# Kernel optimization log

Hardware: AMD Instinct MI355X
Metric: run time of the kernel (lower is better)

Reference implementation:

```python
import jax, jax.numpy as jnp
import numpy as np

N_HEADS = 12
C = 3          # per-head in/hidden/out channels (12/4)
C_PRED = 1     # predictor hidden (4/4)
BN_EPS = 1e-5
COS_EPS = 1e-8
B, H, W = 8, 512, 768


def setup_inputs() -> dict:
    key = jax.random.key(0)
    ks = jax.random.split(key, 22)
    p = lambda k, s: jax.random.normal(k, s, jnp.float32) * 0.1
    return {
        "latent1": jax.random.normal(ks[0], (B, N_HEADS, H, W), jnp.float32),
        "latent2": jax.random.normal(ks[1], (B, N_HEADS, H, W), jnp.float32),
        # projector conv1 + BN
        "W1": p(ks[2], (N_HEADS, C, C)), "b1": p(ks[3], (N_HEADS, C)),
        "g1": 1.0 + p(ks[4], (N_HEADS, C)), "be1": p(ks[5], (N_HEADS, C)),
        # projector conv2 + BN
        "W2": p(ks[6], (N_HEADS, C, C)), "b2": p(ks[7], (N_HEADS, C)),
        "g2": 1.0 + p(ks[8], (N_HEADS, C)), "be2": p(ks[9], (N_HEADS, C)),
        # projector conv3 + BN (no ReLU)
        "W3": p(ks[10], (N_HEADS, C, C)), "b3": p(ks[11], (N_HEADS, C)),
        "g3": 1.0 + p(ks[12], (N_HEADS, C)), "be3": p(ks[13], (N_HEADS, C)),
        # predictor conv1 + BN
        "W4": p(ks[14], (N_HEADS, C_PRED, C)), "b4": p(ks[15], (N_HEADS, C_PRED)),
        "g4": 1.0 + p(ks[16], (N_HEADS, C_PRED)), "be4": p(ks[17], (N_HEADS, C_PRED)),
        # predictor conv2 (no BN)
        "W5": p(ks[18], (N_HEADS, C, C_PRED)), "b5": p(ks[19], (N_HEADS, C)),
    }


def _conv1x1(x, Wk, bk):
    # x: [B, Cin, H, W'], Wk: [Cout, Cin]
    return jnp.einsum('oc,bchw->bohw', Wk, x) + bk[None, :, None, None]


def _bn(x, g, be):
    # training-mode BatchNorm2d: batch statistics over (B, H, W)
    m = x.mean(axis=(0, 2, 3), keepdims=True)
    v = x.var(axis=(0, 2, 3), keepdims=True)  # biased var, as torch BN uses
    return (x - m) * jax.lax.rsqrt(v + BN_EPS) * g[None, :, None, None] + be[None, :, None, None]


def _cos_loss(p, z):
    # -mean(cosine_similarity(p, detach(z), dim=1))
    z = jax.lax.stop_gradient(z)
    dot = jnp.sum(p * z, axis=1)
    npn = jnp.maximum(jnp.sqrt(jnp.sum(p * p, axis=1)), COS_EPS)
    nzn = jnp.maximum(jnp.sqrt(jnp.sum(z * z, axis=1)), COS_EPS)
    return -jnp.mean(dot / (npn * nzn))


def _head_loss(x1, x2, W1, b1, g1, be1, W2, b2, g2, be2, W3, b3, g3, be3,
               W4, b4, g4, be4, W5, b5):
    def proj(x):
        x = jax.nn.relu(_bn(_conv1x1(x, W1, b1), g1, be1))
        x = jax.nn.relu(_bn(_conv1x1(x, W2, b2), g2, be2))
        return _bn(_conv1x1(x, W3, b3), g3, be3)

    def pred(z):
        h = jax.nn.relu(_bn(_conv1x1(z, W4, b4), g4, be4))
        return _conv1x1(h, W5, b5)

    z1, z2 = proj(x1), proj(x2)
    p1, p2 = pred(z1), pred(z2)
    return 0.5 * (_cos_loss(p1, z2) + _cos_loss(p2, z1))


def reference(latent1, latent2, W1, b1, g1, be1, W2, b2, g2, be2,
              W3, b3, g3, be3, W4, b4, g4, be4, W5, b5):
    Bd, Cd, Hd, Wd = latent1.shape
    Wp = Wd // C
    # per-channel view [B, H, W] -> [B, 3, H, W/3]; stack heads on leading axis
    x1 = latent1.reshape(Bd, N_HEADS, C, Hd, Wp).transpose(1, 0, 2, 3, 4)
    x2 = latent2.reshape(Bd, N_HEADS, C, Hd, Wp).transpose(1, 0, 2, 3, 4)
    losses = jax.vmap(_head_loss)(x1, x2, W1, b1, g1, be1, W2, b2, g2, be2,
                                  W3, b3, g3, be3, W4, b4, g4, be4, W5, b5)
    return jnp.sum(losses)
```

## Files before the change

kernel.cpp:

```cpp
#include <hip/hip_runtime.h>
#include <math.h>


constexpr int   NH      = 12;
constexpr int   POS     = 131072;
constexpr int   NB      = 8;
constexpr long long MLL = (long long)NB * POS;
constexpr int   NG      = (int)(MLL / 4);
constexpr int   GX      = 256;
constexpr float COS_EPS = 1e-8f;

template <int K>
__device__ inline void block_reduce_to0(double (&v)[K]) {
#pragma unroll
  for (int off = 32; off > 0; off >>= 1) {
#pragma unroll
    for (int k = 0; k < K; ++k) v[k] += __shfl_down(v[k], off, 64);
  }
  __shared__ double lds[4][K];
  const int lane = threadIdx.x & 63;
  const int wv   = threadIdx.x >> 6;
  if (lane == 0) {
#pragma unroll
    for (int k = 0; k < K; ++k) lds[wv][k] = v[k];
  }
  __syncthreads();
  if (threadIdx.x == 0) {
#pragma unroll
    for (int k = 0; k < K; ++k) v[k] = lds[0][k] + lds[1][k] + lds[2][k] + lds[3][k];
  }
}

__global__ __launch_bounds__(256) void pass1_kernel(
    const float* __restrict__ x1, const float* __restrict__ x2,
    const float* __restrict__ W1, const float* __restrict__ b1,
    double* __restrict__ P1) {
  const int s = blockIdx.y;
  const int n = s >> 1;
  const float* __restrict__ X = (s & 1) ? x2 : x1;

  float w[3][3], bb[3];
#pragma unroll
  for (int o = 0; o < 3; ++o) {
#pragma unroll
    for (int c = 0; c < 3; ++c) w[o][c] = W1[n * 9 + o * 3 + c];
    bb[o] = b1[n * 3 + o];
  }

  float acc[6] = {0.f, 0.f, 0.f, 0.f, 0.f, 0.f};
  for (int g = blockIdx.x * 256 + threadIdx.x; g < NG; g += GX * 256) {
    const int b   = g >> 15;
    const int pos = (g & 32767) << 2;
    const float* base = X + (size_t)((b * NH + n) * 3) * POS + pos;
    const float4 v0 = *(const float4*)(base);
    const float4 v1 = *(const float4*)(base + POS);
    const float4 v2 = *(const float4*)(base + 2 * POS);
    const float* f0 = (const float*)&v0;
    const float* f1 = (const float*)&v1;
    const float* f2 = (const float*)&v2;
#pragma unroll
    for (int j = 0; j < 4; ++j) {
      const float X0 = f0[j], X1 = f1[j], X2 = f2[j];
#pragma unroll
      for (int o = 0; o < 3; ++o) {
        const float y = fmaf(w[o][0], X0, fmaf(w[o][1], X1, fmaf(w[o][2], X2, bb[o])));
        acc[o]     += y;
        acc[3 + o] += y * y;
      }
    }
  }

  double v[6];
#pragma unroll
  for (int k = 0; k < 6; ++k) v[k] = (double)acc[k];
  block_reduce_to0<6>(v);
  if (threadIdx.x == 0) {
    double* dst = P1 + ((size_t)s * GX + blockIdx.x) * 6;
#pragma unroll
    for (int k = 0; k < 6; ++k) dst[k] = v[k];
  }
}

__global__ __launch_bounds__(256) void pass2_kernel(
    const float* __restrict__ x1, const float* __restrict__ x2,
    const float* __restrict__ W1, const float* __restrict__ b1,
    const float* __restrict__ W2, const float* __restrict__ b2,
    const float* __restrict__ derived, double* __restrict__ P2) {
  const int s = blockIdx.y;
  const int n = s >> 1;
  const float* __restrict__ X = (s & 1) ? x2 : x1;

  float w1[3][3], bb1[3], w2[3][3], bb2[3], s1[3], t1[3];
#pragma unroll
  for (int o = 0; o < 3; ++o) {
#pragma unroll
    for (int c = 0; c < 3; ++c) {
      w1[o][c] = W1[n * 9 + o * 3 + c];
      w2[o][c] = W2[n * 9 + o * 3 + c];
    }
    bb1[o] = b1[n * 3 + o];
    bb2[o] = b2[n * 3 + o];
    s1[o]  = derived[s * 20 + o];
    t1[o]  = derived[s * 20 + 3 + o];
  }

  float acc[6] = {0.f, 0.f, 0.f, 0.f, 0.f, 0.f};
  for (int g = blockIdx.x * 256 + threadIdx.x; g < NG; g += GX * 256) {
    const int b   = g >> 15;
    const int pos = (g & 32767) << 2;
    const float* base = X + (size_t)((b * NH + n) * 3) * POS + pos;
    const float4 v0 = *(const float4*)(base);
    const float4 v1 = *(const float4*)(base + POS);
    const float4 v2 = *(const float4*)(base + 2 * POS);
    const float* f0 = (const float*)&v0;
    const float* f1 = (const float*)&v1;
    const float* f2 = (const float*)&v2;
#pragma unroll
    for (int j = 0; j < 4; ++j) {
      const float X0 = f0[j], X1 = f1[j], X2 = f2[j];
      float a[3];
#pragma unroll
      for (int o = 0; o < 3; ++o) {
        const float y = fmaf(w1[o][0], X0, fmaf(w1[o][1], X1, fmaf(w1[o][2], X2, bb1[o])));
        a[o] = fmaxf(0.f, fmaf(s1[o], y, t1[o]));
      }
#pragma unroll
      for (int o = 0; o < 3; ++o) {
        const float y2v = fmaf(w2[o][0], a[0], fmaf(w2[o][1], a[1], fmaf(w2[o][2], a[2], bb2[o])));
        acc[o]     += y2v;
        acc[3 + o] += y2v * y2v;
      }
    }
  }

  double v[6];
#pragma unroll
  for (int k = 0; k < 6; ++k) v[k] = (double)acc[k];
  block_reduce_to0<6>(v);
  if (threadIdx.x == 0) {
    double* dst = P2 + ((size_t)s * GX + blockIdx.x) * 6;
#pragma unroll
    for (int k = 0; k < 6; ++k) dst[k] = v[k];
  }
}

__global__ __launch_bounds__(256) void pass3_kernel(
    const float* __restrict__ x1, const float* __restrict__ x2,
    const float* __restrict__ W1, const float* __restrict__ b1,
    const float* __restrict__ W2, const float* __restrict__ b2,
    const float* __restrict__ W3, const float* __restrict__ b3,
    const float* __restrict__ derived, double* __restrict__ P3) {
  const int s = blockIdx.y;
  const int n = s >> 1;
  const float* __restrict__ X = (s & 1) ? x2 : x1;

  float w1[3][3], bb1[3], w2[3][3], bb2[3], w3[3][3], bb3[3];
  float s1[3], t1[3], s2[3], t2[3];
#pragma unroll
  for (int o = 0; o < 3; ++o) {
#pragma unroll
    for (int c = 0; c < 3; ++c) {
      w1[o][c] = W1[n * 9 + o * 3 + c];
      w2[o][c] = W2[n * 9 + o * 3 + c];
      w3[o][c] = W3[n * 9 + o * 3 + c];
    }
    bb1[o] = b1[n * 3 + o];
    bb2[o] = b2[n * 3 + o];
    bb3[o] = b3[n * 3 + o];
    s1[o]  = derived[s * 20 + o];
    t1[o]  = derived[s * 20 + 3 + o];
    s2[o]  = derived[s * 20 + 6 + o];
    t2[o]  = derived[s * 20 + 9 + o];
  }

  float acc[9] = {0.f, 0.f, 0.f, 0.f, 0.f, 0.f, 0.f, 0.f, 0.f};
  for (int g = blockIdx.x * 256 + threadIdx.x; g < NG; g += GX * 256) {
    const int b   = g >> 15;
    const int pos = (g & 32767) << 2;
    const float* base = X + (size_t)((b * NH + n) * 3) * POS + pos;
    const float4 v0 = *(const float4*)(base);
    const float4 v1 = *(const float4*)(base + POS);
    const float4 v2 = *(const float4*)(base + 2 * POS);
    const float* f0 = (const float*)&v0;
    const float* f1 = (const float*)&v1;
    const float* f2 = (const float*)&v2;
#pragma unroll
    for (int j = 0; j < 4; ++j) {
      const float X0 = f0[j], X1 = f1[j], X2 = f2[j];
      float a[3], a2[3], y3[3];
#pragma unroll
      for (int o = 0; o < 3; ++o) {
        const float y = fmaf(w1[o][0], X0, fmaf(w1[o][1], X1, fmaf(w1[o][2], X2, bb1[o])));
        a[o] = fmaxf(0.f, fmaf(s1[o], y, t1[o]));
      }
#pragma unroll
      for (int o = 0; o < 3; ++o) {
        const float y = fmaf(w2[o][0], a[0], fmaf(w2[o][1], a[1], fmaf(w2[o][2], a[2], bb2[o])));
        a2[o] = fmaxf(0.f, fmaf(s2[o], y, t2[o]));
      }
#pragma unroll
      for (int o = 0; o < 3; ++o) {
        y3[o] = fmaf(w3[o][0], a2[0], fmaf(w3[o][1], a2[1], fmaf(w3[o][2], a2[2], bb3[o])));
        acc[o]     += y3[o];
        acc[3 + o] += y3[o] * y3[o];
      }
      acc[6] += y3[0] * y3[1];
      acc[7] += y3[0] * y3[2];
      acc[8] += y3[1] * y3[2];
    }
  }

  double v[9];
#pragma unroll
  for (int k = 0; k < 9; ++k) v[k] = (double)acc[k];
  block_reduce_to0<9>(v);
  if (threadIdx.x == 0) {
    double* dst = P3 + ((size_t)s * GX + blockIdx.x) * 9;
#pragma unroll
    for (int k = 0; k < 9; ++k) dst[k] = v[k];
  }
}

__global__ __launch_bounds__(256) void bn_stats_reduce(
    const double* __restrict__ partials,
    const float* __restrict__ gamma, const float* __restrict__ beta,
    float* __restrict__ derived, int doff) {
  const int s = blockIdx.x;
  const int t = threadIdx.x;
  double v[6];
  const double* p = partials + ((size_t)s * GX + t) * 6;
#pragma unroll
  for (int k = 0; k < 6; ++k) v[k] = p[k];
  block_reduce_to0<6>(v);
  if (t == 0) {
    const int n = s >> 1;
#pragma unroll
    for (int c = 0; c < 3; ++c) {
      const double mean = v[c] / (double)MLL;
      const double var  = v[3 + c] / (double)MLL - mean * mean;
      const double sc   = (double)gamma[n * 3 + c] / sqrt(var + 1e-5);
      derived[s * 20 + doff + c]     = (float)sc;
      derived[s * 20 + doff + 3 + c] = (float)((double)beta[n * 3 + c] - mean * sc);
    }
  }
}

__global__ __launch_bounds__(256) void bn_stats3_reduce(
    const double* __restrict__ partials,
    const float* __restrict__ g3, const float* __restrict__ be3,
    const float* __restrict__ W4, const float* __restrict__ b4,
    const float* __restrict__ g4, const float* __restrict__ be4,
    float* __restrict__ derived) {
  const int s = blockIdx.x;
  const int t = threadIdx.x;
  double v[9];
  const double* p = partials + ((size_t)s * GX + t) * 9;
#pragma unroll
  for (int k = 0; k < 9; ++k) v[k] = p[k];
  block_reduce_to0<9>(v);
  if (t == 0) {
    const int n = s >> 1;
    double mean[3] = {v[0] / (double)MLL, v[1] / (double)MLL, v[2] / (double)MLL};
    double E[3][3];
    E[0][0] = v[3] / (double)MLL;
    E[1][1] = v[4] / (double)MLL;
    E[2][2] = v[5] / (double)MLL;
    E[0][1] = E[1][0] = v[6] / (double)MLL;
    E[0][2] = E[2][0] = v[7] / (double)MLL;
    E[1][2] = E[2][1] = v[8] / (double)MLL;
    double cov[3][3];
    for (int i = 0; i < 3; ++i)
      for (int j = 0; j < 3; ++j) cov[i][j] = E[i][j] - mean[i] * mean[j];

    double s3[3], t3[3];
    for (int c = 0; c < 3; ++c) {
      s3[c] = (double)g3[n * 3 + c] / sqrt(cov[c][c] + 1e-5);
      t3[c] = (double)be3[n * 3 + c] - mean[c] * s3[c];
      derived[s * 20 + 12 + c] = (float)s3[c];
      derived[s * 20 + 15 + c] = (float)t3[c];
    }
    double u[3], dd = (double)b4[n];
    for (int c = 0; c < 3; ++c) {
      u[c] = (double)W4[n * 3 + c] * s3[c];
      dd += (double)W4[n * 3 + c] * t3[c];
    }
    double m4 = dd;
    for (int c = 0; c < 3; ++c) m4 += u[c] * mean[c];
    double v4 = 0.0;
    for (int i = 0; i < 3; ++i)
      for (int j = 0; j < 3; ++j) v4 += u[i] * u[j] * cov[i][j];
    const double s4 = (double)g4[n] / sqrt(v4 + 1e-5);
    derived[s * 20 + 18] = (float)s4;
    derived[s * 20 + 19] = (float)((double)be4[n] - m4 * s4);
  }
}

__device__ inline void fwd_chain(
    const float w1[3][3], const float bb1[3],
    const float w2[3][3], const float bb2[3],
    const float w3[3][3], const float bb3[3],
    const float w4[3], float b4s, const float w5[3], const float b5v[3],
    const float* __restrict__ S,
    float X0, float X1, float X2, float z[3], float p[3]) {
  float a[3], a2[3];
#pragma unroll
  for (int o = 0; o < 3; ++o) {
    const float y = fmaf(w1[o][0], X0, fmaf(w1[o][1], X1, fmaf(w1[o][2], X2, bb1[o])));
    a[o] = fmaxf(0.f, fmaf(S[o], y, S[3 + o]));
  }
#pragma unroll
  for (int o = 0; o < 3; ++o) {
    const float y = fmaf(w2[o][0], a[0], fmaf(w2[o][1], a[1], fmaf(w2[o][2], a[2], bb2[o])));
    a2[o] = fmaxf(0.f, fmaf(S[6 + o], y, S[9 + o]));
  }
  float y4 = b4s;
#pragma unroll
  for (int o = 0; o < 3; ++o) {
    const float y = fmaf(w3[o][0], a2[0], fmaf(w3[o][1], a2[1], fmaf(w3[o][2], a2[2], bb3[o])));
    z[o] = fmaf(S[12 + o], y, S[15 + o]);
    y4 = fmaf(w4[o], z[o], y4);
  }
  const float h = fmaxf(0.f, fmaf(S[18], y4, S[19]));
#pragma unroll
  for (int o = 0; o < 3; ++o) p[o] = fmaf(w5[o], h, b5v[o]);
}

__global__ __launch_bounds__(256) void pass_loss_kernel(
    const float* __restrict__ x1, const float* __restrict__ x2,
    const float* __restrict__ W1, const float* __restrict__ b1,
    const float* __restrict__ W2, const float* __restrict__ b2,
    const float* __restrict__ W3, const float* __restrict__ b3,
    const float* __restrict__ W4, const float* __restrict__ b4,
    const float* __restrict__ W5, const float* __restrict__ b5,
    const float* __restrict__ derived, double* __restrict__ PL) {
  const int n = blockIdx.y;

  float w1[3][3], bb1[3], w2[3][3], bb2[3], w3[3][3], bb3[3];
  float w4[3], b4s, w5[3], b5v[3];
#pragma unroll
  for (int o = 0; o < 3; ++o) {
#pragma unroll
    for (int c = 0; c < 3; ++c) {
      w1[o][c] = W1[n * 9 + o * 3 + c];
      w2[o][c] = W2[n * 9 + o * 3 + c];
      w3[o][c] = W3[n * 9 + o * 3 + c];
    }
    bb1[o] = b1[n * 3 + o];
    bb2[o] = b2[n * 3 + o];
    bb3[o] = b3[n * 3 + o];
    w4[o]  = W4[n * 3 + o];
    w5[o]  = W5[n * 3 + o];
    b5v[o] = b5[n * 3 + o];
  }
  b4s = b4[n];

  float S0[20], S1[20];
#pragma unroll
  for (int k = 0; k < 20; ++k) {
    S0[k] = derived[(n * 2 + 0) * 20 + k];
    S1[k] = derived[(n * 2 + 1) * 20 + k];
  }

  float acc = 0.f;
  for (int g = blockIdx.x * 256 + threadIdx.x; g < NG; g += GX * 256) {
    const int b   = g >> 15;
    const int pos = (g & 32767) << 2;
    const size_t off = (size_t)((b * NH + n) * 3) * POS + pos;
    const float4 u0 = *(const float4*)(x1 + off);
    const float4 u1 = *(const float4*)(x1 + off + POS);
    const float4 u2 = *(const float4*)(x1 + off + 2 * POS);
    const float4 q0 = *(const float4*)(x2 + off);
    const float4 q1 = *(const float4*)(x2 + off + POS);
    const float4 q2 = *(const float4*)(x2 + off + 2 * POS);
    const float* a0 = (const float*)&u0;
    const float* a1 = (const float*)&u1;
    const float* a2p = (const float*)&u2;
    const float* c0 = (const float*)&q0;
    const float* c1 = (const float*)&q1;
    const float* c2 = (const float*)&q2;
#pragma unroll
    for (int j = 0; j < 4; ++j) {
      float z1[3], p1[3], z2[3], p2[3];
      fwd_chain(w1, bb1, w2, bb2, w3, bb3, w4, b4s, w5, b5v, S0,
                a0[j], a1[j], a2p[j], z1, p1);
      fwd_chain(w1, bb1, w2, bb2, w3, bb3, w4, b4s, w5, b5v, S1,
                c0[j], c1[j], c2[j], z2, p2);

      const float d12 = p1[0] * z2[0] + p1[1] * z2[1] + p1[2] * z2[2];
      const float pp1 = p1[0] * p1[0] + p1[1] * p1[1] + p1[2] * p1[2];
      const float zz2 = z2[0] * z2[0] + z2[1] * z2[1] + z2[2] * z2[2];
      const float c12 = d12 / (fmaxf(sqrtf(pp1), COS_EPS) * fmaxf(sqrtf(zz2), COS_EPS));

      const float d21 = p2[0] * z1[0] + p2[1] * z1[1] + p2[2] * z1[2];
      const float pp2 = p2[0] * p2[0] + p2[1] * p2[1] + p2[2] * p2[2];
      const float zz1 = z1[0] * z1[0] + z1[1] * z1[1] + z1[2] * z1[2];
      const float c21 = d21 / (fmaxf(sqrtf(pp2), COS_EPS) * fmaxf(sqrtf(zz1), COS_EPS));

      acc += c12 + c21;
    }
  }

  double v[1] = {(double)acc};
  block_reduce_to0<1>(v);
  if (threadIdx.x == 0) PL[(size_t)n * GX + blockIdx.x] = v[0];
}

__global__ __launch_bounds__(256) void finalize_kernel(
    const double* __restrict__ PL, float* __restrict__ out) {
  double v[1] = {0.0};
#pragma unroll
  for (int h = 0; h < NH; ++h) v[0] += PL[(size_t)h * GX + threadIdx.x];
  block_reduce_to0<1>(v);
  if (threadIdx.x == 0) out[0] = (float)(-0.5 * v[0] / (double)MLL);
}

extern "C" void kernel_launch(void* const* d_in, const int* in_sizes, int n_in,
                              void* d_out, int out_size, void* d_ws, size_t ws_size,
                              hipStream_t stream) {
  const float* x1  = (const float*)d_in[0];
  const float* x2  = (const float*)d_in[1];
  const float* W1  = (const float*)d_in[2];
  const float* b1  = (const float*)d_in[3];
  const float* g1  = (const float*)d_in[4];
  const float* be1 = (const float*)d_in[5];
  const float* W2  = (const float*)d_in[6];
  const float* b2  = (const float*)d_in[7];
  const float* g2  = (const float*)d_in[8];
  const float* be2 = (const float*)d_in[9];
  const float* W3  = (const float*)d_in[10];
  const float* b3  = (const float*)d_in[11];
  const float* g3  = (const float*)d_in[12];
  const float* be3 = (const float*)d_in[13];
  const float* W4  = (const float*)d_in[14];
  const float* b4  = (const float*)d_in[15];
  const float* g4  = (const float*)d_in[16];
  const float* be4 = (const float*)d_in[17];
  const float* W5  = (const float*)d_in[18];
  const float* b5  = (const float*)d_in[19];

  double* dws = (double*)d_ws;
  double* P1 = dws;
  double* P2 = dws + 24 * GX * 6;
  double* P3 = dws + 2 * 24 * GX * 6;
  double* PL = dws + 2 * 24 * GX * 6 + 24 * GX * 9;
  float* derived = (float*)(dws + 2 * 24 * GX * 6 + 24 * GX * 9 + NH * GX);

  const dim3 blk(256);
  pass1_kernel<<<dim3(GX, 24), blk, 0, stream>>>(x1, x2, W1, b1, P1);
  bn_stats_reduce<<<24, 256, 0, stream>>>(P1, g1, be1, derived, 0);
  pass2_kernel<<<dim3(GX, 24), blk, 0, stream>>>(x1, x2, W1, b1, W2, b2, derived, P2);
  bn_stats_reduce<<<24, 256, 0, stream>>>(P2, g2, be2, derived, 6);
  pass3_kernel<<<dim3(GX, 24), blk, 0, stream>>>(x1, x2, W1, b1, W2, b2, W3, b3, derived, P3);
  bn_stats3_reduce<<<24, 256, 0, stream>>>(P3, g3, be3, W4, b4, g4, be4, derived);
  pass_loss_kernel<<<dim3(GX, NH), blk, 0, stream>>>(x1, x2, W1, b1, W2, b2, W3, b3,
                                                     W4, b4, W5, b5, derived, PL);
  finalize_kernel<<<1, 256, 0, stream>>>(PL, (float*)d_out);
}
```

Before: 536.7 us.

## Cache inputs as bf16 in workspace and derive layer-1 BN stats analytically

The first pass now accumulates the input channel means and covariances and computes the BN1 statistics analytically from W1. It also writes a bf16 copy of both inputs into the workspace when the workspace is large enough. Passes B, C and D then read the half-size bf16 copy instead of the fp32 inputs, cutting memory traffic in the three later passes. The grid is remapped to contiguous per-(batch, head) chunks. In exchange it adds a bf16 write pass and bf16 rounding error in the later BN statistics and the loss, plus a large workspace requirement.

After: 511.4 us. 1.05x faster.

```diff
diff --git a/kernel.cpp b/kernel.cpp
--- a/kernel.cpp
+++ b/kernel.cpp
@@ -1,14 +1,23 @@
 #include <hip/hip_runtime.h>
 #include <math.h>
 
+
+typedef unsigned short ushort_t;
+typedef unsigned int uint_t;
 
 constexpr int   NH      = 12;
 constexpr int   POS     = 131072;
 constexpr int   NB      = 8;
 constexpr long long MLL = (long long)NB * POS;
-constexpr int   NG      = (int)(MLL / 4);
-constexpr int   GX      = 256;
+constexpr int   CSPAN   = POS / 16;
+constexpr int   SBLK    = 128;
+constexpr int   NTOT    = NB * NH * 3 * POS;
 constexpr float COS_EPS = 1e-8f;
+
+constexpr size_t XB_BYTES   = (size_t)NTOT * 2;
+constexpr size_t DBL_COUNT  = (size_t)24 * SBLK * 9 + (size_t)24 * SBLK * 6 +
+                              (size_t)24 * SBLK * 9 + (size_t)12 * SBLK;
+constexpr size_t NEED_BYTES = 2 * XB_BYTES + DBL_COUNT * 8 + 480 * 4;
 
 template <int K>
 __device__ inline void block_reduce_to0(double (&v)[K]) {
@@ -31,64 +40,145 @@
   }
 }
 
-__global__ __launch_bounds__(256) void pass1_kernel(
+__device__ inline uint_t pack2bf(float lo, float hi) {
+  uint_t ul = __float_as_uint(lo);
+  uint_t uh = __float_as_uint(hi);
+  ul = ul + 0x7FFFu + ((ul >> 16) & 1u);
+  uh = uh + 0x7FFFu + ((uh >> 16) & 1u);
+  return (ul >> 16) | (uh & 0xFFFF0000u);
+}
+
+__device__ inline void unpack8(const uint4 v, float (&f)[8]) {
+  const uint_t w0 = v.x, w1 = v.y, w2 = v.z, w3 = v.w;
+  f[0] = __uint_as_float(w0 << 16); f[1] = __uint_as_float(w0 & 0xFFFF0000u);
+  f[2] = __uint_as_float(w1 << 16); f[3] = __uint_as_float(w1 & 0xFFFF0000u);
+  f[4] = __uint_as_float(w2 << 16); f[5] = __uint_as_float(w2 & 0xFFFF0000u);
+  f[6] = __uint_as_float(w3 << 16); f[7] = __uint_as_float(w3 & 0xFFFF0000u);
+}
+
+template <bool BF16>
+__device__ inline void load_ch3(const float* __restrict__ X,
+                                const ushort_t* __restrict__ XB,
+                                size_t eoff, float (&f)[3][8]) {
+#pragma unroll
+  for (int c = 0; c < 3; ++c) {
+    const size_t a = eoff + (size_t)c * POS;
+    if constexpr (BF16) {
+      const uint4 v = *(const uint4*)(XB + a);
+      unpack8(v, f[c]);
+    } else {
+      const float4 u0 = *(const float4*)(X + a);
+      const float4 u1 = *(const float4*)(X + a + 4);
+      f[c][0] = u0.x; f[c][1] = u0.y; f[c][2] = u0.z; f[c][3] = u0.w;
+      f[c][4] = u1.x; f[c][5] = u1.y; f[c][6] = u1.z; f[c][7] = u1.w;
+    }
+  }
+}
+
+template <bool STORE>
+__global__ __launch_bounds__(256) void passA_kernel(
     const float* __restrict__ x1, const float* __restrict__ x2,
-    const float* __restrict__ W1, const float* __restrict__ b1,
-    double* __restrict__ P1) {
-  const int s = blockIdx.y;
+    ushort_t* __restrict__ xb1, ushort_t* __restrict__ xb2,
+    double* __restrict__ P0) {
+  const int u = blockIdx.y;
+  const int s = u % 24;
+  const int b = u / 24;
   const int n = s >> 1;
   const float* __restrict__ X = (s & 1) ? x2 : x1;
-
-  float w[3][3], bb[3];
-#pragma unroll
-  for (int o = 0; o < 3; ++o) {
-#pragma unroll
-    for (int c = 0; c < 3; ++c) w[o][c] = W1[n * 9 + o * 3 + c];
-    bb[o] = b1[n * 3 + o];
-  }
-
-  float acc[6] = {0.f, 0.f, 0.f, 0.f, 0.f, 0.f};
-  for (int g = blockIdx.x * 256 + threadIdx.x; g < NG; g += GX * 256) {
-    const int b   = g >> 15;
-    const int pos = (g & 32767) << 2;
-    const float* base = X + (size_t)((b * NH + n) * 3) * POS + pos;
-    const float4 v0 = *(const float4*)(base);
-    const float4 v1 = *(const float4*)(base + POS);
-    const float4 v2 = *(const float4*)(base + 2 * POS);
-    const float* f0 = (const float*)&v0;
-    const float* f1 = (const float*)&v1;
-    const float* f2 = (const float*)&v2;
+  ushort_t* __restrict__ XB = (s & 1) ? xb2 : xb1;
+  const size_t off0 = (size_t)((b * NH + n) * 3) * POS + (size_t)blockIdx.x * CSPAN;
+
+  float acc[9] = {0.f, 0.f, 0.f, 0.f, 0.f, 0.f, 0.f, 0.f, 0.f};
+#pragma unroll
+  for (int i = 0; i < 8; ++i) {
+    const int idx = i * 1024 + threadIdx.x * 4;
+    float4 v[3];
+#pragma unroll
+    for (int c = 0; c < 3; ++c)
+      v[c] = *(const float4*)(X + off0 + (size_t)c * POS + idx);
+    if constexpr (STORE) {
+#pragma unroll
+      for (int c = 0; c < 3; ++c) {
+        uint2 h;
+        h.x = pack2bf(v[c].x, v[c].y);
+        h.y = pack2bf(v[c].z, v[c].w);
+        *(uint2*)(XB + off0 + (size_t)c * POS + idx) = h;
+      }
+    }
+    const float* f0 = (const float*)&v[0];
+    const float* f1 = (const float*)&v[1];
+    const float* f2 = (const float*)&v[2];
 #pragma unroll
     for (int j = 0; j < 4; ++j) {
       const float X0 = f0[j], X1 = f1[j], X2 = f2[j];
-#pragma unroll
-      for (int o = 0; o < 3; ++o) {
-        const float y = fmaf(w[o][0], X0, fmaf(w[o][1], X1, fmaf(w[o][2], X2, bb[o])));
-        acc[o]     += y;
-        acc[3 + o] += y * y;
-      }
-    }
-  }
-
-  double v[6];
-#pragma unroll
-  for (int k = 0; k < 6; ++k) v[k] = (double)acc[k];
-  block_reduce_to0<6>(v);
+      acc[0] += X0;      acc[1] += X1;      acc[2] += X2;
+      acc[3] += X0 * X0; acc[4] += X1 * X1; acc[5] += X2 * X2;
+      acc[6] += X0 * X1; acc[7] += X0 * X2; acc[8] += X1 * X2;
+    }
+  }
+
+  double v9[9];
+#pragma unroll
+  for (int k = 0; k < 9; ++k) v9[k] = (double)acc[k];
+  block_reduce_to0<9>(v9);
   if (threadIdx.x == 0) {
-    double* dst = P1 + ((size_t)s * GX + blockIdx.x) * 6;
-#pragma unroll
-    for (int k = 0; k < 6; ++k) dst[k] = v[k];
-  }
-}
-
-__global__ __launch_bounds__(256) void pass2_kernel(
+    double* dst = P0 + ((size_t)s * SBLK + b * 16 + blockIdx.x) * 9;
+#pragma unroll
+    for (int k = 0; k < 9; ++k) dst[k] = v9[k];
+  }
+}
+
+__global__ __launch_bounds__(256) void bn_statsA_kernel(
+    const double* __restrict__ P0, const float* __restrict__ W1,
+    const float* __restrict__ b1, const float* __restrict__ g1,
+    const float* __restrict__ be1, float* __restrict__ derived) {
+  const int s = blockIdx.x;
+  const int t = threadIdx.x;
+  const int n = s >> 1;
+  double v[9] = {0, 0, 0, 0, 0, 0, 0, 0, 0};
+  if (t < SBLK) {
+    const double* p = P0 + ((size_t)s * SBLK + t) * 9;
+#pragma unroll
+    for (int k = 0; k < 9; ++k) v[k] = p[k];
+  }
+  block_reduce_to0<9>(v);
+  if (t == 0) {
+    const double M = (double)MLL;
+    double m[3] = {v[0] / M, v[1] / M, v[2] / M};
+    double C00 = v[3] / M - m[0] * m[0];
+    double C11 = v[4] / M - m[1] * m[1];
+    double C22 = v[5] / M - m[2] * m[2];
+    double C01 = v[6] / M - m[0] * m[1];
+    double C02 = v[7] / M - m[0] * m[2];
+    double C12 = v[8] / M - m[1] * m[2];
+    for (int o = 0; o < 3; ++o) {
+      const double w0 = W1[n * 9 + o * 3 + 0];
+      const double w1v = W1[n * 9 + o * 3 + 1];
+      const double w2v = W1[n * 9 + o * 3 + 2];
+      const double my = w0 * m[0] + w1v * m[1] + w2v * m[2] + (double)b1[n * 3 + o];
+      const double vy = w0 * w0 * C00 + w1v * w1v * C11 + w2v * w2v * C22 +
+                        2.0 * (w0 * w1v * C01 + w0 * w2v * C02 + w1v * w2v * C12);
+      const double sc = (double)g1[n * 3 + o] / sqrt(vy + 1e-5);
+      derived[s * 20 + o]     = (float)sc;
+      derived[s * 20 + 3 + o] = (float)((double)be1[n * 3 + o] - my * sc);
+    }
+  }
+}
+
+template <bool BF16>
+__global__ __launch_bounds__(256) void passB_kernel(
     const float* __restrict__ x1, const float* __restrict__ x2,
+    const ushort_t* __restrict__ xb1, const ushort_t* __restrict__ xb2,
     const float* __restrict__ W1, const float* __restrict__ b1,
     const float* __restrict__ W2, const float* __restrict__ b2,
     const float* __restrict__ derived, double* __restrict__ P2) {
-  const int s = blockIdx.y;
+  const int u = blockIdx.y;
+  const int s = u % 24;
+  const int b = u / 24;
   const int n = s >> 1;
   const float* __restrict__ X = (s & 1) ? x2 : x1;
+  const ushort_t* __restrict__ XB = (s & 1) ? xb2 : xb1;
+  const size_t off0 = (size_t)((b * NH + n) * 3) * POS + (size_t)blockIdx.x * CSPAN;
 
   float w1[3][3], bb1[3], w2[3][3], bb2[3], s1[3], t1[3];
 #pragma unroll
@@ -105,19 +195,14 @@
   }
 
   float acc[6] = {0.f, 0.f, 0.f, 0.f, 0.f, 0.f};
-  for (int g = blockIdx.x * 256 + threadIdx.x; g < NG; g += GX * 256) {
-    const int b   = g >> 15;
-    const int pos = (g & 32767) << 2;
-    const float* base = X + (size_t)((b * NH + n) * 3) * POS + pos;
-    const float4 v0 = *(const float4*)(base);
-    const float4 v1 = *(const float4*)(base + POS);
-    const float4 v2 = *(const float4*)(base + 2 * POS);
-    const float* f0 = (const float*)&v0;
-    const float* f1 = (const float*)&v1;
-    const float* f2 = (const float*)&v2;
-#pragma unroll
-    for (int j = 0; j < 4; ++j) {
-      const float X0 = f0[j], X1 = f1[j], X2 = f2[j];
+#pragma unroll 2
+  for (int i = 0; i < 4; ++i) {
+    const size_t eoff = off0 + i * 2048 + threadIdx.x * 8;
+    float f[3][8];
+    load_ch3<BF16>(X, XB, eoff, f);
+#pragma unroll
+    for (int j = 0; j < 8; ++j) {
+      const float X0 = f[0][j], X1 = f[1][j], X2 = f[2][j];
       float a[3];
 #pragma unroll
       for (int o = 0; o < 3; ++o) {
@@ -138,21 +223,52 @@
   for (int k = 0; k < 6; ++k) v[k] = (double)acc[k];
   block_reduce_to0<6>(v);
   if (threadIdx.x == 0) {
-    double* dst = P2 + ((size_t)s * GX + blockIdx.x) * 6;
+    double* dst = P2 + ((size_t)s * SBLK + b * 16 + blockIdx.x) * 6;
 #pragma unroll
     for (int k = 0; k < 6; ++k) dst[k] = v[k];
   }
 }
 
-__global__ __launch_bounds__(256) void pass3_kernel(
+__global__ __launch_bounds__(256) void bn_statsB_kernel(
+    const double* __restrict__ P2, const float* __restrict__ gamma,
+    const float* __restrict__ beta, float* __restrict__ derived) {
+  const int s = blockIdx.x;
+  const int t = threadIdx.x;
+  const int n = s >> 1;
+  double v[6] = {0, 0, 0, 0, 0, 0};
+  if (t < SBLK) {
+    const double* p = P2 + ((size_t)s * SBLK + t) * 6;
+#pragma unroll
+    for (int k = 0; k < 6; ++k) v[k] = p[k];
+  }
+  block_reduce_to0<6>(v);
+  if (t == 0) {
+#pragma unroll
+    for (int c = 0; c < 3; ++c) {
+      const double mean = v[c] / (double)MLL;
+      const double var  = v[3 + c] / (double)MLL - mean * mean;
+      const double sc   = (double)gamma[n * 3 + c] / sqrt(var + 1e-5);
+      derived[s * 20 + 6 + c] = (float)sc;
+      derived[s * 20 + 9 + c] = (float)((double)beta[n * 3 + c] - mean * sc);
+    }
+  }
+}
+
+template <bool BF16>
+__global__ __launch_bounds__(256) void passC_kernel(
     const float* __restrict__ x1, const float* __restrict__ x2,
+    const ushort_t* __restrict__ xb1, const ushort_t* __restrict__ xb2,
     const float* __restrict__ W1, const float* __restrict__ b1,
     const float* __restrict__ W2, const float* __restrict__ b2,
     const float* __restrict__ W3, const float* __restrict__ b3,
     const float* __restrict__ derived, double* __restrict__ P3) {
-  const int s = blockIdx.y;
+  const int u = blockIdx.y;
+  const int s = u % 24;
+  const int b = u / 24;
   const int n = s >> 1;
   const float* __restrict__ X = (s & 1) ? x2 : x1;
+  const ushort_t* __restrict__ XB = (s & 1) ? xb2 : xb1;
+  const size_t off0 = (size_t)((b * NH + n) * 3) * POS + (size_t)blockIdx.x * CSPAN;
 
   float w1[3][3], bb1[3], w2[3][3], bb2[3], w3[3][3], bb3[3];
   float s1[3], t1[3], s2[3], t2[3];
@@ -174,19 +290,14 @@
   }
 
   float acc[9] = {0.f, 0.f, 0.f, 0.f, 0.f, 0.f, 0.f, 0.f, 0.f};
-  for (int g = blockIdx.x * 256 + threadIdx.x; g < NG; g += GX * 256) {
-    const int b   = g >> 15;
-    const int pos = (g & 32767) << 2;
-    const float* base = X + (size_t)((b * NH + n) * 3) * POS + pos;
-    const float4 v0 = *(const float4*)(base);
-    const float4 v1 = *(const float4*)(base + POS);
-    const float4 v2 = *(const float4*)(base + 2 * POS);
-    const float* f0 = (const float*)&v0;
-    const float* f1 = (const float*)&v1;
-    const float* f2 = (const float*)&v2;
-#pragma unroll
-    for (int j = 0; j < 4; ++j) {
-      const float X0 = f0[j], X1 = f1[j], X2 = f2[j];
+#pragma unroll 2
+  for (int i = 0; i < 4; ++i) {
+    const size_t eoff = off0 + i * 2048 + threadIdx.x * 8;
+    float f[3][8];
+    load_ch3<BF16>(X, XB, eoff, f);
+#pragma unroll
+    for (int j = 0; j < 8; ++j) {
+      const float X0 = f[0][j], X1 = f[1][j], X2 = f[2][j];
       float a[3], a2[3], y3[3];
 #pragma unroll
       for (int o = 0; o < 3; ++o) {
@@ -215,62 +326,37 @@
   for (int k = 0; k < 9; ++k) v[k] = (double)acc[k];
   block_reduce_to0<9>(v);
   if (threadIdx.x == 0) {
-    double* dst = P3 + ((size_t)s * GX + blockIdx.x) * 9;
+    double* dst = P3 + ((size_t)s * SBLK + b * 16 + blockIdx.x) * 9;
 #pragma unroll
     for (int k = 0; k < 9; ++k) dst[k] = v[k];
   }
 }
 
-__global__ __launch_bounds__(256) void bn_stats_reduce(
-    const double* __restrict__ partials,
-    const float* __restrict__ gamma, const float* __restrict__ beta,
-    float* __restrict__ derived, int doff) {
+__global__ __launch_bounds__(256) void bn_statsC_kernel(
+    const double* __restrict__ P3, const float* __restrict__ g3,
+    const float* __restrict__ be3, const float* __restrict__ W4,
+    const float* __restrict__ b4, const float* __restrict__ g4,
+    const float* __restrict__ be4, float* __restrict__ derived) {
   const int s = blockIdx.x;
   const int t = threadIdx.x;
-  double v[6];
-  const double* p = partials + ((size_t)s * GX + t) * 6;
-#pragma unroll
-  for (int k = 0; k < 6; ++k) v[k] = p[k];
-  block_reduce_to0<6>(v);
-  if (t == 0) {
-    const int n = s >> 1;
-#pragma unroll
-    for (int c = 0; c < 3; ++c) {
-      const double mean = v[c] / (double)MLL;
-      const double var  = v[3 + c] / (double)MLL - mean * mean;
-      const double sc   = (double)gamma[n * 3 + c] / sqrt(var + 1e-5);
-      derived[s * 20 + doff + c]     = (float)sc;
-      derived[s * 20 + doff + 3 + c] = (float)((double)beta[n * 3 + c] - mean * sc);
-    }
-  }
-}
-
-__global__ __launch_bounds__(256) void bn_stats3_reduce(
-    const double* __restrict__ partials,
-    const float* __restrict__ g3, const float* __restrict__ be3,
-    const float* __restrict__ W4, const float* __restrict__ b4,
-    const float* __restrict__ g4, const float* __restrict__ be4,
-    float* __restrict__ derived) {
-  const int s = blockIdx.x;
-  const int t = threadIdx.x;
-  double v[9];
-  const double* p = partials + ((size_t)s * GX + t) * 9;
-#pragma unroll
-  for (int k = 0; k < 9; ++k) v[k] = p[k];
+  const int n = s >> 1;
+  double v[9] = {0, 0, 0, 0, 0, 0, 0, 0, 0};
+  if (t < SBLK) {
+    const double* p = P3 + ((size_t)s * SBLK + t) * 9;
+#pragma unroll
+    for (int k = 0; k < 9; ++k) v[k] = p[k];
+  }
   block_reduce_to0<9>(v);
   if (t == 0) {
-    const int n = s >> 1;
-    double mean[3] = {v[0] / (double)MLL, v[1] / (double)MLL, v[2] / (double)MLL};
-    double E[3][3];
-    E[0][0] = v[3] / (double)MLL;
-    E[1][1] = v[4] / (double)MLL;
-    E[2][2] = v[5] / (double)MLL;
-    E[0][1] = E[1][0] = v[6] / (double)MLL;
-    E[0][2] = E[2][0] = v[7] / (double)MLL;
-    E[1][2] = E[2][1] = v[8] / (double)MLL;
+    const double M = (double)MLL;
+    double mean[3] = {v[0] / M, v[1] / M, v[2] / M};
     double cov[3][3];
-    for (int i = 0; i < 3; ++i)
-      for (int j = 0; j < 3; ++j) cov[i][j] = E[i][j] - mean[i] * mean[j];
+    cov[0][0] = v[3] / M - mean[0] * mean[0];
+    cov[1][1] = v[4] / M - mean[1] * mean[1];
+    cov[2][2] = v[5] / M - mean[2] * mean[2];
+    cov[0][1] = cov[1][0] = v[6] / M - mean[0] * mean[1];
+    cov[0][2] = cov[2][0] = v[7] / M - mean[0] * mean[2];
+    cov[1][2] = cov[2][1] = v[8] / M - mean[1] * mean[2];
 
     double s3[3], t3[3];
     for (int c = 0; c < 3; ++c) {
@@ -300,8 +386,7 @@
     const float w2[3][3], const float bb2[3],
     const float w3[3][3], const float bb3[3],
     const float w4[3], float b4s, const float w5[3], const float b5v[3],
-    const float* __restrict__ S,
-    float X0, float X1, float X2, float z[3], float p[3]) {
+    const float* S, float X0, float X1, float X2, float z[3], float p[3]) {
   float a[3], a2[3];
 #pragma unroll
   for (int o = 0; o < 3; ++o) {
@@ -325,15 +410,20 @@
   for (int o = 0; o < 3; ++o) p[o] = fmaf(w5[o], h, b5v[o]);
 }
 
-__global__ __launch_bounds__(256) void pass_loss_kernel(
+template <bool BF16>
+__global__ __launch_bounds__(256) void passD_kernel(
     const float* __restrict__ x1, const float* __restrict__ x2,
+    const ushort_t* __restrict__ xb1, const ushort_t* __restrict__ xb2,
     const float* __restrict__ W1, const float* __restrict__ b1,
     const float* __restrict__ W2, const float* __restrict__ b2,
     const float* __restrict__ W3, const float* __restrict__ b3,
     const float* __restrict__ W4, const float* __restrict__ b4,
     const float* __restrict__ W5, const float* __restrict__ b5,
     const float* __restrict__ derived, double* __restrict__ PL) {
-  const int n = blockIdx.y;
+  const int u = blockIdx.y;
+  const int n = u % 12;
+  const int b = u / 12;
+  const size_t off0 = (size_t)((b * NH + n) * 3) * POS + (size_t)blockIdx.x * CSPAN;
 
   float w1[3][3], bb1[3], w2[3][3], bb2[3], w3[3][3], bb3[3];
   float w4[3], b4s, w5[3], b5v[3];
@@ -362,29 +452,18 @@
   }
 
   float acc = 0.f;
-  for (int g = blockIdx.x * 256 + threadIdx.x; g < NG; g += GX * 256) {
-    const int b   = g >> 15;
-    const int pos = (g & 32767) << 2;
-    const size_t off = (size_t)((b * NH + n) * 3) * POS + pos;
-    const float4 u0 = *(const float4*)(x1 + off);
-    const float4 u1 = *(const float4*)(x1 + off + POS);
-    const float4 u2 = *(const float4*)(x1 + off + 2 * POS);
-    const float4 q0 = *(const float4*)(x2 + off);
-    const float4 q1 = *(const float4*)(x2 + off + POS);
-    const float4 q2 = *(const float4*)(x2 + off + 2 * POS);
-    const float* a0 = (const float*)&u0;
-    const float* a1 = (const float*)&u1;
-    const float* a2p = (const float*)&u2;
-    const float* c0 = (const float*)&q0;
-    const float* c1 = (const float*)&q1;
-    const float* c2 = (const float*)&q2;
-#pragma unroll
-    for (int j = 0; j < 4; ++j) {
+  for (int i = 0; i < 4; ++i) {
+    const size_t eoff = off0 + i * 2048 + threadIdx.x * 8;
+    float fA[3][8], fB[3][8];
+    load_ch3<BF16>(x1, xb1, eoff, fA);
+    load_ch3<BF16>(x2, xb2, eoff, fB);
+#pragma unroll
+    for (int j = 0; j < 8; ++j) {
       float z1[3], p1[3], z2[3], p2[3];
       fwd_chain(w1, bb1, w2, bb2, w3, bb3, w4, b4s, w5, b5v, S0,
-                a0[j], a1[j], a2p[j], z1, p1);
+                fA[0][j], fA[1][j], fA[2][j], z1, p1);
       fwd_chain(w1, bb1, w2, bb2, w3, bb3, w4, b4s, w5, b5v, S1,
-                c0[j], c1[j], c2[j], z2, p2);
+                fB[0][j], fB[1][j], fB[2][j], z2, p2);
 
       const float d12 = p1[0] * z2[0] + p1[1] * z2[1] + p1[2] * z2[2];
       const float pp1 = p1[0] * p1[0] + p1[1] * p1[1] + p1[2] * p1[2];
@@ -402,14 +481,13 @@
 
   double v[1] = {(double)acc};
   block_reduce_to0<1>(v);
-  if (threadIdx.x == 0) PL[(size_t)n * GX + blockIdx.x] = v[0];
+  if (threadIdx.x == 0) PL[(size_t)n * SBLK + b * 16 + blockIdx.x] = v[0];
 }
 
 __global__ __launch_bounds__(256) void finalize_kernel(
     const double* __restrict__ PL, float* __restrict__ out) {
   double v[1] = {0.0};
-#pragma unroll
-  for (int h = 0; h < NH; ++h) v[0] += PL[(size_t)h * GX + threadIdx.x];
+  for (int k = threadIdx.x; k < 12 * SBLK; k += 256) v[0] += PL[k];
   block_reduce_to0<1>(v);
   if (threadIdx.x == 0) out[0] = (float)(-0.5 * v[0] / (double)MLL);
 }
@@ -438,21 +516,50 @@
   const float* W5  = (const float*)d_in[18];
   const float* b5  = (const float*)d_in[19];
 
-  double* dws = (double*)d_ws;
-  double* P1 = dws;
-  double* P2 = dws + 24 * GX * 6;
-  double* P3 = dws + 2 * 24 * GX * 6;
-  double* PL = dws + 2 * 24 * GX * 6 + 24 * GX * 9;
-  float* derived = (float*)(dws + 2 * 24 * GX * 6 + 24 * GX * 9 + NH * GX);
+  const bool big = ws_size >= NEED_BYTES;
+  ushort_t* xb1 = nullptr;
+  ushort_t* xb2 = nullptr;
+  double* dbase;
+  if (big) {
+    xb1 = (ushort_t*)d_ws;
+    xb2 = xb1 + NTOT;
+    dbase = (double*)(xb2 + NTOT);
+  } else {
+    dbase = (double*)d_ws;
+  }
+  double* P0 = dbase;
+  double* P2 = P0 + (size_t)24 * SBLK * 9;
+  double* P3 = P2 + (size_t)24 * SBLK * 6;
+  double* PL = P3 + (size_t)24 * SBLK * 9;
+  float* derived = (float*)(PL + 12 * SBLK);
 
   const dim3 blk(256);
-  pass1_kernel<<<dim3(GX, 24), blk, 0, stream>>>(x1, x2, W1, b1, P1);
-  bn_stats_reduce<<<24, 256, 0, stream>>>(P1, g1, be1, derived, 0);
-  pass2_kernel<<<dim3(GX, 24), blk, 0, stream>>>(x1, x2, W1, b1, W2, b2, derived, P2);
-  bn_stats_reduce<<<24, 256, 0, stream>>>(P2, g2, be2, derived, 6);
-  pass3_kernel<<<dim3(GX, 24), blk, 0, stream>>>(x1, x2, W1, b1, W2, b2, W3, b3, derived, P3);
-  bn_stats3_reduce<<<24, 256, 0, stream>>>(P3, g3, be3, W4, b4, g4, be4, derived);
-  pass_loss_kernel<<<dim3(GX, NH), blk, 0, stream>>>(x1, x2, W1, b1, W2, b2, W3, b3,
-                                                     W4, b4, W5, b5, derived, PL);
-  finalize_kernel<<<1, 256, 0, stream>>>(PL, (float*)d_out);
-}
+  const dim3 gA(16, 192);
+  const dim3 gD(16, 96);
+
+  if (big) {
+    passA_kernel<true><<<gA, blk, 0, stream>>>(x1, x2, xb1, xb2, P0);
+    bn_statsA_kernel<<<24, blk, 0, stream>>>(P0, W1, b1, g1, be1, derived);
+    passB_kernel<true><<<gA, blk, 0, stream>>>(x1, x2, xb1, xb2, W1, b1, W2, b2,
+                                               derived, P2);
+    bn_statsB_kernel<<<24, blk, 0, stream>>>(P2, g2, be2, derived);
+    passC_kernel<true><<<gA, blk, 0, stream>>>(x1, x2, xb1, xb2, W1, b1, W2, b2,
+                                               W3, b3, derived, P3);
+    bn_statsC_kernel<<<24, blk, 0, stream>>>(P3, g3, be3, W4, b4, g4, be4, derived);
+    passD_kernel<true><<<gD, blk, 0, stream>>>(x1, x2, xb1, xb2, W1, b1, W2, b2,
+                                               W3, b3, W4, b4, W5, b5, derived, PL);
+  } else {
+    passA_kernel<false><<<gA, blk, 0, stream>>>(x1, x2, nullptr, nullptr, P0);
+    bn_statsA_kernel<<<24, blk, 0, stream>>>(P0, W1, b1, g1, be1, derived);
+    passB_kernel<false><<<gA, blk, 0, stream>>>(x1, x2, nullptr, nullptr, W1, b1,
+                                                W2, b2, derived, P2);
+    bn_statsB_kernel<<<24, blk, 0, stream>>>(P2, g2, be2, derived);
+    passC_kernel<false><<<gA, blk, 0, stream>>>(x1, x2, nullptr, nullptr, W1, b1,
+                                                W2, b2, W3, b3, derived, P3);
+    bn_statsC_kernel<<<24, blk, 0, stream>>>(P3, g3, be3, W4, b4, g4, be4, derived);
+    passD_kernel<false><<<gD, blk, 0, stream>>>(x1, x2, nullptr, nullptr, W1, b1,
+                                                W2, b2, W3, b3, W4, b4, W5, b5,
+                                                derived, PL);
+  }
+  finalize_kernel<<<1, blk, 0, stream>>>(PL, (float*)d_out);
+}
```
